# Performance work log

Measured on AMD Instinct MI355X. Metric: run time of the kernel, lower is better.

Reference implementation:

```python
import jax, jax.numpy as jnp
import numpy as np

B, C, W = 8, 128, 4096
REDUCTION = 8
D = C // REDUCTION  # 16


def setup_inputs() -> dict:
    key = jax.random.key(0)
    ks = jax.random.split(key, 7)
    scale = 0.05
    return {
        "x": jax.random.normal(ks[0], (B, C, W), dtype=jnp.float32),
        "Wq": jax.random.normal(ks[1], (D, C), dtype=jnp.float32) * scale,
        "bq": jax.random.normal(ks[2], (D,), dtype=jnp.float32) * scale,
        "Wk": jax.random.normal(ks[3], (D, C), dtype=jnp.float32) * scale,
        "bk": jax.random.normal(ks[4], (D,), dtype=jnp.float32) * scale,
        "Wv": jax.random.normal(ks[5], (C, C), dtype=jnp.float32) * scale,
        "bv": jax.random.normal(ks[6], (C,), dtype=jnp.float32) * scale,
    }


def reference(x, Wq, bq, Wk, bk, Wv, bv):
    # 1x1 Conv1d == per-position linear over channel axis
    q = jnp.einsum('dc,bcw->bdw', Wq, x) + bq[None, :, None]   # [B, D, W]
    k = jnp.einsum('dc,bcw->bdw', Wk, x) + bk[None, :, None]   # [B, D, W]
    v = jnp.einsum('oc,bcw->bow', Wv, x) + bv[None, :, None]   # [B, C, W]
    scale = D ** (-0.5)
    # scores[b,i,j] = q[b,:,i] . k[b,:,j]
    scores = jnp.einsum('bdi,bdj->bij', q, k) * scale          # [B, W, W]
    attn = jax.nn.softmax(scores, axis=-1)
    # torch.bmm(value, attn): context[b,c,w] = sum_j v[b,c,j] * attn[b,j,w]
    context = jnp.einsum('bcj,bjw->bcw', v, attn)              # [B, C, W]
    return context + x
```

## Files before the change

kernel.cpp:

```cpp
#include <hip/hip_runtime.h>

#define B_ 8
#define C_ 128
#define W_ 4096
#define D_ 16
#define SCALE2 0.3606737602222409f

typedef short bf16x8 __attribute__((ext_vector_type(8)));
typedef float f32x4 __attribute__((ext_vector_type(4)));
typedef float f32x16 __attribute__((ext_vector_type(16)));

__device__ __forceinline__ unsigned short f2bf(float f) {
    unsigned int u = __float_as_uint(f);
    u += 0x7fffu + ((u >> 16) & 1u);
    return (unsigned short)(u >> 16);
}
__device__ __forceinline__ float bf2f(unsigned short h) {
    return __uint_as_float(((unsigned int)h) << 16);
}
__device__ __forceinline__ unsigned int pk2bf(float lo, float hi) {
    return __builtin_amdgcn_perm(__float_as_uint(hi), __float_as_uint(lo), 0x07060302u);
}
__device__ __forceinline__ bf16x8 u4_to_bf8(unsigned int a, unsigned int b,
                                            unsigned int c, unsigned int d) {
    union { uint4 u; bf16x8 v; } t;
    t.u = make_uint4(a, b, c, d);
    return t.v;
}
__device__ __forceinline__ bf16x8 uint4_as_bf8(uint4 u) {
    union { uint4 u; bf16x8 v; } t;
    t.u = u;
    return t.v;
}
__device__ __forceinline__ bf16x8 exp2pack8(f32x16 s, int r0) {
    return u4_to_bf8(
        pk2bf(__builtin_amdgcn_exp2f(s[r0+0]), __builtin_amdgcn_exp2f(s[r0+1])),
        pk2bf(__builtin_amdgcn_exp2f(s[r0+2]), __builtin_amdgcn_exp2f(s[r0+3])),
        pk2bf(__builtin_amdgcn_exp2f(s[r0+4]), __builtin_amdgcn_exp2f(s[r0+5])),
        pk2bf(__builtin_amdgcn_exp2f(s[r0+6]), __builtin_amdgcn_exp2f(s[r0+7])));
}
__device__ __forceinline__ int xswz(int j, int c8) {
    return c8 ^ (j & 7) ^ ((j >> 3) & 7);
}

__global__ __launch_bounds__(256) void prep(
    const float* __restrict__ Wq, const float* __restrict__ Wk, const float* __restrict__ Wv,
    unsigned short* __restrict__ Wvbf, unsigned short* __restrict__ Wqkbf)
{
    int g = blockIdx.x * 256 + threadIdx.x;
    const float* src; unsigned short* dst; float sc = 1.0f;
    if (g < 4096)      { src = Wv + g * 4;            dst = Wvbf + g * 4; }
    else if (g < 4608) { int t = g - 4096; src = Wq + t * 4; dst = Wqkbf + t * 4; sc = SCALE2; }
    else               { int t = g - 4608; src = Wk + t * 4; dst = Wqkbf + 2048 + t * 4; }
    float4 v = *(const float4*)src;
    unsigned short h[4] = {f2bf(v.x * sc), f2bf(v.y * sc), f2bf(v.z * sc), f2bf(v.w * sc)};
    *(ushort4*)dst = *(ushort4*)h;
}

__global__ __launch_bounds__(256) void proj(
    const float* __restrict__ x, const unsigned short* __restrict__ Wvbf,
    const unsigned short* __restrict__ Wqkbf,
    const float* __restrict__ bqp, const float* __restrict__ bkp, const float* __restrict__ bvp,
    unsigned short* __restrict__ qws2, unsigned short* __restrict__ kws2,
    unsigned short* __restrict__ vws2)
{
    __shared__ unsigned short xbf[32 * 128];
    __shared__ unsigned short outs[128 * 36];
    __shared__ unsigned short qk_s[2][32][24];

    int b  = blockIdx.x & 7;
    int j0 = (blockIdx.x >> 3) * 32;
    int jt = j0 >> 5;
    int tid = threadIdx.x;
    int wid = tid >> 6, lane = tid & 63, n = lane & 15, q4 = lane >> 4;

    {
        unsigned int* xbf32 = (unsigned int*)xbf;
#pragma unroll
        for (int i = 0; i < 8; i++) {
            int p = tid + 256 * i;
            int c2 = p >> 5;
            int j  = p & 31;
            const float* xp = x + (size_t)(b * C_ + 2 * c2) * W_ + j0 + j;
            float lo = xp[0];
            float hi = xp[W_];
            xbf32[j * 64 + xswz(j, c2 >> 2) * 4 + (c2 & 3)] = pk2bf(lo, hi);
        }
    }
    __syncthreads();

    const f32x4 zero = {0.f, 0.f, 0.f, 0.f};
    f32x4 accv[2][2]; f32x4 accqk = zero;
#pragma unroll
    for (int os = 0; os < 2; os++)
#pragma unroll
        for (int js = 0; js < 2; js++) accv[os][js] = zero;

    int isK = wid >> 1;
    int jsm = wid & 1;

#pragma unroll
    for (int kk = 0; kk < 128; kk += 32) {
        bf16x8 av[2], aqkf, bx[2];
#pragma unroll
        for (int os = 0; os < 2; os++)
            av[os] = *(const bf16x8*)(Wvbf + (wid * 32 + os * 16 + n) * 128 + kk + q4 * 8);
        aqkf = *(const bf16x8*)(Wqkbf + (isK * 16 + n) * 128 + kk + q4 * 8);
#pragma unroll
        for (int js = 0; js < 2; js++) {
            int j = js * 16 + n;
            bx[js] = *(const bf16x8*)&xbf[j * 128 + xswz(j, (kk >> 3) + q4) * 8];
        }
#pragma unroll
        for (int os = 0; os < 2; os++)
#pragma unroll
            for (int js = 0; js < 2; js++)
                accv[os][js] = __builtin_amdgcn_mfma_f32_16x16x32_bf16(av[os], bx[js], accv[os][js], 0, 0, 0);
        accqk = __builtin_amdgcn_mfma_f32_16x16x32_bf16(aqkf, bx[jsm], accqk, 0, 0, 0);
    }

    {
        int pos = jsm * 16 + n;
        const float* bias = isK ? bkp : bqp;
        float bsc = isK ? 1.0f : SCALE2;
#pragma unroll
        for (int r = 0; r < 4; r++)
            qk_s[isK][pos][q4 * 4 + r] = f2bf(accqk[r] + bias[q4 * 4 + r] * bsc);
    }

    float bvv[2][4];
#pragma unroll
    for (int os = 0; os < 2; os++)
#pragma unroll
        for (int r = 0; r < 4; r++) bvv[os][r] = bvp[wid * 32 + os * 16 + q4 * 4 + r];
#pragma unroll
    for (int os = 0; os < 2; os++)
#pragma unroll
        for (int js = 0; js < 2; js++)
#pragma unroll
            for (int r = 0; r < 4; r++) {
                int c = wid * 32 + os * 16 + q4 * 4 + r;
                int j = js * 16 + n;
                outs[c * 36 + j] = f2bf(accv[os][js][r] + bvv[os][r]);
            }
    __syncthreads();

    if (tid < 128) {
        int qk = tid >> 6, hh = (tid >> 5) & 1, jl = tid & 31;
        uint4 v = *(const uint4*)&qk_s[qk][jl][hh * 8];
        unsigned short* dst = (qk ? kws2 : qws2)
            + (size_t)(b * 128 + jt) * 512 + hh * 256 + jl * 8;
        *(uint4*)dst = v;
    }
#pragma unroll
    for (int rep = 0; rep < 2; rep++) {
        int t = tid + rep * 256;
        int c = t & 127, sel = t >> 7;
        int jb = (sel >> 1) * 16 + (sel & 1) * 4;
        uint2 lo = *(const uint2*)&outs[c * 36 + jb];
        uint2 hi = *(const uint2*)&outs[c * 36 + jb + 8];
        *(uint4*)(vws2 + ((size_t)(b * 128 + jt) * 4 + sel) * 1024 + c * 8) =
            make_uint4(lo.x, lo.y, hi.x, hi.y);
    }
}

__global__ __launch_bounds__(256) void row_stats(
    const unsigned short* __restrict__ qws2, const unsigned short* __restrict__ kws2,
    float* __restrict__ rlp)
{
    int blk = blockIdx.x;
    int b = blk & 7;
    int j0 = ((blk >> 3) & 31) * 128;
    int wsp = blk >> 8;
    int tid = threadIdx.x;
    int wid = tid >> 6, lane = tid & 63, wl = lane & 31, h = lane >> 5;

    const unsigned short* qb = qws2 + (size_t)b * 65536;
    const unsigned short* kb = kws2 + (size_t)b * 65536;
    int jt = (j0 >> 5) + wid;

    bf16x8 aq = *(const bf16x8*)(qb + (size_t)jt * 512 + h * 256 + wl * 8);
    f32x16 zero16 = {0.f,0.f,0.f,0.f,0.f,0.f,0.f,0.f,0.f,0.f,0.f,0.f,0.f,0.f,0.f,0.f};

    float lt[16];
#pragma unroll
    for (int r = 0; r < 16; r++) lt[r] = 0.f;

    bf16x8 bkc = *(const bf16x8*)(kb + (size_t)(wsp * 32) * 512 + h * 256 + wl * 8);
    for (int t = 0; t < 32; t++) {
        f32x16 s = __builtin_amdgcn_mfma_f32_32x32x16_bf16(aq, bkc, zero16, 0, 0, 0);
        int tn = wsp * 32 + ((t + 1) & 31);
        bkc = *(const bf16x8*)(kb + (size_t)tn * 512 + h * 256 + wl * 8);
#pragma unroll
        for (int r = 0; r < 16; r++) lt[r] += __builtin_amdgcn_exp2f(s[r]);
    }
#pragma unroll
    for (int mask = 1; mask < 32; mask <<= 1)
#pragma unroll
        for (int r = 0; r < 16; r++) lt[r] += __shfl_xor(lt[r], mask, 64);
    if (wl == 0) {
#pragma unroll
        for (int g = 0; g < 4; g++) {
            f32x4 v = {lt[4*g+0], lt[4*g+1], lt[4*g+2], lt[4*g+3]};
            *(f32x4*)(rlp + (size_t)wsp * 32768 + (size_t)b * W_ + j0 + wid * 32 + 4 * h + 8 * g) = v;
        }
    }
}

__global__ __launch_bounds__(256) void finl(const float* __restrict__ rlp,
                                            float* __restrict__ rls)
{
    int g = blockIdx.x * 256 + threadIdx.x;
    float l = rlp[g] + rlp[32768 + g] + rlp[65536 + g] + rlp[98304 + g];
    rls[g] = 1.0f / l;
}

__global__ __launch_bounds__(256) void vscale(unsigned short* __restrict__ vws2,
                                              const float* __restrict__ rls)
{
    int g = blockIdx.x * 256 + threadIdx.x;
    int hh = (g >> 7) & 1, kf = (g >> 8) & 1, jt = (g >> 9) & 127, b = g >> 16;
    int jb = jt * 32 + kf * 16 + 4 * hh;
    const float* rp = rls + (size_t)b * W_ + jb;
    float4 r0 = *(const float4*)rp;
    float4 r1 = *(const float4*)(rp + 8);
    uint4 v = *(const uint4*)(vws2 + (size_t)g * 8);
    unsigned int o0 = pk2bf(bf2f((unsigned short)(v.x & 0xffffu)) * r0.x,
                            bf2f((unsigned short)(v.x >> 16))     * r0.y);
    unsigned int o1 = pk2bf(bf2f((unsigned short)(v.y & 0xffffu)) * r0.z,
                            bf2f((unsigned short)(v.y >> 16))     * r0.w);
    unsigned int o2 = pk2bf(bf2f((unsigned short)(v.z & 0xffffu)) * r1.x,
                            bf2f((unsigned short)(v.z >> 16))     * r1.y);
    unsigned int o3 = pk2bf(bf2f((unsigned short)(v.w & 0xffffu)) * r1.z,
                            bf2f((unsigned short)(v.w >> 16))     * r1.w);
    *(uint4*)(vws2 + (size_t)g * 8) = make_uint4(o0, o1, o2, o3);
}

__global__ __launch_bounds__(256, 2) void attn_out(
    const float* __restrict__ x, const unsigned short* __restrict__ qws2,
    const unsigned short* __restrict__ kws2, const unsigned short* __restrict__ vws2,
    float* __restrict__ out)
{
    __shared__ float red[2][128 * 68];

    int b  = blockIdx.x & 7;
    int w0 = (blockIdx.x >> 3) * 64;
    int tid = threadIdx.x;
    int wid = tid >> 6, lane = tid & 63, wl = lane & 31, h = lane >> 5;

    const unsigned short* qb  = qws2 + (size_t)b * 65536;
    const unsigned short* kb  = kws2 + (size_t)b * 65536;
    const unsigned short* vtb = vws2 + (size_t)b * 524288;

    bf16x8 bk0 = *(const bf16x8*)(kb + (size_t)((w0 >> 5) + 0) * 512 + h * 256 + wl * 8);
    bf16x8 bk1 = *(const bf16x8*)(kb + (size_t)((w0 >> 5) + 1) * 512 + h * 256 + wl * 8);

    f32x16 zero16 = {0.f,0.f,0.f,0.f,0.f,0.f,0.f,0.f,0.f,0.f,0.f,0.f,0.f,0.f,0.f,0.f};
    f32x16 acc[4][2];
#pragma unroll
    for (int mt = 0; mt < 4; mt++)
#pragma unroll
        for (int nt = 0; nt < 2; nt++) acc[mt][nt] = zero16;

    const int qoff = h * 256 + wl * 8;

    bf16x8 aq = *(const bf16x8*)(qb + (size_t)(wid) * 512 + qoff);
    uint4 vf[4][2];
#pragma unroll
    for (int mt = 0; mt < 4; mt++)
#pragma unroll
        for (int kf = 0; kf < 2; kf++)
            vf[mt][kf] = *(const uint4*)(vtb + (size_t)wid * 4096 + kf * 2048 + h * 1024 + (mt * 32 + wl) * 8);
    f32x16 s0 = __builtin_amdgcn_mfma_f32_32x32x16_bf16(aq, bk0, zero16, 0, 0, 0);
    f32x16 s1 = __builtin_amdgcn_mfma_f32_32x32x16_bf16(aq, bk1, zero16, 0, 0, 0);
    aq = *(const bf16x8*)(qb + (size_t)(4 + wid) * 512 + qoff);
    bf16x8 bfrag[2][2];
    bfrag[0][0] = exp2pack8(s0, 0); bfrag[1][0] = exp2pack8(s0, 8);
    bfrag[0][1] = exp2pack8(s1, 0); bfrag[1][1] = exp2pack8(s1, 8);

    for (int it = 0; it < 32; it++) {
        int jtn = ((it + 1) & 31) * 4 + wid;
        uint4 vfn[4][2];
#pragma unroll
        for (int mt = 0; mt < 4; mt++)
#pragma unroll
            for (int kf = 0; kf < 2; kf++)
                vfn[mt][kf] = *(const uint4*)(vtb + (size_t)jtn * 4096 + kf * 2048 + h * 1024 + (mt * 32 + wl) * 8);
#pragma unroll
        for (int mt = 0; mt < 4; mt++)
#pragma unroll
            for (int kf = 0; kf < 2; kf++) {
                bf16x8 af = uint4_as_bf8(vf[mt][kf]);
#pragma unroll
                for (int nt = 0; nt < 2; nt++)
                    acc[mt][nt] = __builtin_amdgcn_mfma_f32_32x32x16_bf16(af, bfrag[kf][nt], acc[mt][nt], 0, 0, 0);
            }
        s0 = __builtin_amdgcn_mfma_f32_32x32x16_bf16(aq, bk0, zero16, 0, 0, 0);
        s1 = __builtin_amdgcn_mfma_f32_32x32x16_bf16(aq, bk1, zero16, 0, 0, 0);
        aq = *(const bf16x8*)(qb + (size_t)(((it + 2) & 31) * 4 + wid) * 512 + qoff);
        bfrag[0][0] = exp2pack8(s0, 0); bfrag[1][0] = exp2pack8(s0, 8);
        bfrag[0][1] = exp2pack8(s1, 0); bfrag[1][1] = exp2pack8(s1, 8);
#pragma unroll
        for (int mt = 0; mt < 4; mt++)
#pragma unroll
            for (int kf = 0; kf < 2; kf++) vf[mt][kf] = vfn[mt][kf];
    }

#define WRITE_TILE(BUF)                                                           \
    {                                                                             \
        float* _b = (BUF);                                                        \
        _Pragma("unroll") for (int mt = 0; mt < 4; mt++)                          \
        _Pragma("unroll") for (int nt = 0; nt < 2; nt++)                          \
        _Pragma("unroll") for (int r = 0; r < 16; r++)                            \
            _b[(mt * 32 + (r & 3) + 8 * (r >> 2) + 4 * h) * 68 + nt * 32 + wl] = acc[mt][nt][r]; \
    }
#define ADD_TILE(BUF)                                                             \
    {                                                                             \
        const float* _b = (BUF);                                                  \
        _Pragma("unroll") for (int mt = 0; mt < 4; mt++)                          \
        _Pragma("unroll") for (int nt = 0; nt < 2; nt++)                          \
        _Pragma("unroll") for (int r = 0; r < 16; r++)                            \
            acc[mt][nt][r] += _b[(mt * 32 + (r & 3) + 8 * (r >> 2) + 4 * h) * 68 + nt * 32 + wl]; \
    }
    if (wid >= 2) WRITE_TILE(red[wid - 2]);
    __syncthreads();
    if (wid < 2) ADD_TILE(red[wid]);
    __syncthreads();
    if (wid == 1) WRITE_TILE(red[0]);
    __syncthreads();
    if (wid == 0) { ADD_TILE(red[0]); WRITE_TILE(red[0]); }
    __syncthreads();
#undef WRITE_TILE
#undef ADD_TILE

#pragma unroll
    for (int u = 0; u < 8; u++) {
        int k = tid + 256 * u;
        int c = k >> 4, wseg = (k & 15) * 4;
        size_t gidx = (size_t)(b * C_ + c) * W_ + w0 + wseg;
        float4 xv = *(const float4*)(x + gidx);
        const float* s = &red[0][c * 68 + wseg];
        float4 o = make_float4(s[0] + xv.x, s[1] + xv.y, s[2] + xv.z, s[3] + xv.w);
        *(float4*)(out + gidx) = o;
    }
}

extern "C" void kernel_launch(void* const* d_in, const int* in_sizes, int n_in,
                              void* d_out, int out_size, void* d_ws, size_t ws_size,
                              hipStream_t stream)
{
    const float* x  = (const float*)d_in[0];
    const float* Wq = (const float*)d_in[1];
    const float* bq = (const float*)d_in[2];
    const float* Wk = (const float*)d_in[3];
    const float* bk = (const float*)d_in[4];
    const float* Wv = (const float*)d_in[5];
    const float* bv = (const float*)d_in[6];
    float* out = (float*)d_out;

    unsigned short* qws2 = (unsigned short*)d_ws;
    unsigned short* kws2 = qws2 + (size_t)524288;
    unsigned short* vws2 = kws2 + (size_t)524288;
    unsigned short* Wvbf = vws2 + (size_t)4194304;
    unsigned short* Wqkbf = Wvbf + 16384;
    float* rlp = (float*)(Wqkbf + 4096);
    float* rls = rlp + 131072;

    prep<<<20, 256, 0, stream>>>(Wq, Wk, Wv, Wvbf, Wqkbf);
    proj<<<1024, 256, 0, stream>>>(x, Wvbf, Wqkbf, bq, bk, bv, qws2, kws2, vws2);
    row_stats<<<1024, 256, 0, stream>>>(qws2, kws2, rlp);
    finl<<<128, 256, 0, stream>>>(rlp, rls);
    vscale<<<2048, 256, 0, stream>>>(vws2, rls);
    attn_out<<<512, 256, 0, stream>>>(x, qws2, kws2, vws2, out);
}
```

Baseline: 160.1 us.

## Split attn_out work across 8 waves sharing P tiles via LDS

After: 158.3 us. No clear change (-1.2%).

```diff
diff --git a/kernel.cpp b/kernel.cpp
--- a/kernel.cpp
+++ b/kernel.cpp
@@ -32,8 +32,8 @@
     t.u = u;
     return t.v;
 }
-__device__ __forceinline__ bf16x8 exp2pack8(f32x16 s, int r0) {
-    return u4_to_bf8(
+__device__ __forceinline__ uint4 exp2pkq(f32x16 s, int r0) {
+    return make_uint4(
         pk2bf(__builtin_amdgcn_exp2f(s[r0+0]), __builtin_amdgcn_exp2f(s[r0+1])),
         pk2bf(__builtin_amdgcn_exp2f(s[r0+2]), __builtin_amdgcn_exp2f(s[r0+3])),
         pk2bf(__builtin_amdgcn_exp2f(s[r0+4]), __builtin_amdgcn_exp2f(s[r0+5])),
@@ -236,112 +236,105 @@
     *(uint4*)(vws2 + (size_t)g * 8) = make_uint4(o0, o1, o2, o3);
 }
 
-__global__ __launch_bounds__(256, 2) void attn_out(
+__global__ __launch_bounds__(512, 4) void attn_out(
     const float* __restrict__ x, const unsigned short* __restrict__ qws2,
     const unsigned short* __restrict__ kws2, const unsigned short* __restrict__ vws2,
     float* __restrict__ out)
 {
-    __shared__ float red[2][128 * 68];
+    __shared__ uint4 p_lds[2][1024];
+    __shared__ float red[128 * 68];
 
     int b  = blockIdx.x & 7;
     int w0 = (blockIdx.x >> 3) * 64;
     int tid = threadIdx.x;
     int wid = tid >> 6, lane = tid & 63, wl = lane & 31, h = lane >> 5;
+    int cq = wid >> 1, kh = wid & 1;
 
     const unsigned short* qb  = qws2 + (size_t)b * 65536;
     const unsigned short* kb  = kws2 + (size_t)b * 65536;
-    const unsigned short* vtb = vws2 + (size_t)b * 524288;
-
-    bf16x8 bk0 = *(const bf16x8*)(kb + (size_t)((w0 >> 5) + 0) * 512 + h * 256 + wl * 8);
-    bf16x8 bk1 = *(const bf16x8*)(kb + (size_t)((w0 >> 5) + 1) * 512 + h * 256 + wl * 8);
+    const uint4* vtb4 = (const uint4*)(vws2 + (size_t)b * 524288) + h * 128 + (cq * 32 + wl);
+    const int qoff = h * 256 + wl * 8;
+
+    bf16x8 bk = *(const bf16x8*)(kb + (size_t)((w0 >> 5) + kh) * 512 + h * 256 + wl * 8);
 
     f32x16 zero16 = {0.f,0.f,0.f,0.f,0.f,0.f,0.f,0.f,0.f,0.f,0.f,0.f,0.f,0.f,0.f,0.f};
-    f32x16 acc[4][2];
-#pragma unroll
-    for (int mt = 0; mt < 4; mt++)
-#pragma unroll
-        for (int nt = 0; nt < 2; nt++) acc[mt][nt] = zero16;
-
-    const int qoff = h * 256 + wl * 8;
-
-    bf16x8 aq = *(const bf16x8*)(qb + (size_t)(wid) * 512 + qoff);
-    uint4 vf[4][2];
-#pragma unroll
-    for (int mt = 0; mt < 4; mt++)
-#pragma unroll
-        for (int kf = 0; kf < 2; kf++)
-            vf[mt][kf] = *(const uint4*)(vtb + (size_t)wid * 4096 + kf * 2048 + h * 1024 + (mt * 32 + wl) * 8);
-    f32x16 s0 = __builtin_amdgcn_mfma_f32_32x32x16_bf16(aq, bk0, zero16, 0, 0, 0);
-    f32x16 s1 = __builtin_amdgcn_mfma_f32_32x32x16_bf16(aq, bk1, zero16, 0, 0, 0);
-    aq = *(const bf16x8*)(qb + (size_t)(4 + wid) * 512 + qoff);
-    bf16x8 bfrag[2][2];
-    bfrag[0][0] = exp2pack8(s0, 0); bfrag[1][0] = exp2pack8(s0, 8);
-    bfrag[0][1] = exp2pack8(s1, 0); bfrag[1][1] = exp2pack8(s1, 8);
-
+    f32x16 acc[2];
+    acc[0] = zero16; acc[1] = zero16;
+
+    const int wbase = cq * 256 + h * 64 + kh * 32 + wl;
+    const int rbase = kh * 512 + h * 64 + wl;
+
+    bf16x8 aq = *(const bf16x8*)(qb + (size_t)cq * 512 + qoff);
+    uint4 vf[4];
+#pragma unroll
+    for (int kf = 0; kf < 4; kf++)
+        vf[kf] = vtb4[(size_t)(kh * 4 + kf) * 256];
+    {
+        f32x16 s = __builtin_amdgcn_mfma_f32_32x32x16_bf16(aq, bk, zero16, 0, 0, 0);
+        aq = *(const bf16x8*)(qb + (size_t)(4 + cq) * 512 + qoff);
+        p_lds[0][wbase]       = exp2pkq(s, 0);
+        p_lds[0][wbase + 128] = exp2pkq(s, 8);
+    }
+    __syncthreads();
+
+#pragma unroll 2
     for (int it = 0; it < 32; it++) {
-        int jtn = ((it + 1) & 31) * 4 + wid;
-        uint4 vfn[4][2];
-#pragma unroll
-        for (int mt = 0; mt < 4; mt++)
-#pragma unroll
-            for (int kf = 0; kf < 2; kf++)
-                vfn[mt][kf] = *(const uint4*)(vtb + (size_t)jtn * 4096 + kf * 2048 + h * 1024 + (mt * 32 + wl) * 8);
-#pragma unroll
-        for (int mt = 0; mt < 4; mt++)
-#pragma unroll
-            for (int kf = 0; kf < 2; kf++) {
-                bf16x8 af = uint4_as_bf8(vf[mt][kf]);
-#pragma unroll
-                for (int nt = 0; nt < 2; nt++)
-                    acc[mt][nt] = __builtin_amdgcn_mfma_f32_32x32x16_bf16(af, bfrag[kf][nt], acc[mt][nt], 0, 0, 0);
+        int cur = it & 1, nxt = cur ^ 1;
+        uint4 vfn[4];
+#pragma unroll
+        for (int kf = 0; kf < 4; kf++) {
+            int kg = ((it + 1) & 31) * 8 + kh * 4 + kf;
+            vfn[kf] = vtb4[(size_t)kg * 256];
+        }
+        f32x16 s = __builtin_amdgcn_mfma_f32_32x32x16_bf16(aq, bk, zero16, 0, 0, 0);
+        aq = *(const bf16x8*)(qb + (size_t)(((it + 2) & 31) * 4 + cq) * 512 + qoff);
+        p_lds[nxt][wbase]       = exp2pkq(s, 0);
+        p_lds[nxt][wbase + 128] = exp2pkq(s, 8);
+        __builtin_amdgcn_s_setprio(1);
+#pragma unroll
+        for (int kf = 0; kf < 4; kf++) {
+            bf16x8 af = uint4_as_bf8(vf[kf]);
+#pragma unroll
+            for (int nt = 0; nt < 2; nt++) {
+                bf16x8 bp = uint4_as_bf8(p_lds[cur][rbase + kf * 128 + nt * 32]);
+                acc[nt] = __builtin_amdgcn_mfma_f32_32x32x16_bf16(af, bp, acc[nt], 0, 0, 0);
             }
-        s0 = __builtin_amdgcn_mfma_f32_32x32x16_bf16(aq, bk0, zero16, 0, 0, 0);
-        s1 = __builtin_amdgcn_mfma_f32_32x32x16_bf16(aq, bk1, zero16, 0, 0, 0);
-        aq = *(const bf16x8*)(qb + (size_t)(((it + 2) & 31) * 4 + wid) * 512 + qoff);
-        bfrag[0][0] = exp2pack8(s0, 0); bfrag[1][0] = exp2pack8(s0, 8);
-        bfrag[0][1] = exp2pack8(s1, 0); bfrag[1][1] = exp2pack8(s1, 8);
-#pragma unroll
-        for (int mt = 0; mt < 4; mt++)
-#pragma unroll
-            for (int kf = 0; kf < 2; kf++) vf[mt][kf] = vfn[mt][kf];
-    }
-
-#define WRITE_TILE(BUF)                                                           \
-    {                                                                             \
-        float* _b = (BUF);                                                        \
-        _Pragma("unroll") for (int mt = 0; mt < 4; mt++)                          \
-        _Pragma("unroll") for (int nt = 0; nt < 2; nt++)                          \
-        _Pragma("unroll") for (int r = 0; r < 16; r++)                            \
-            _b[(mt * 32 + (r & 3) + 8 * (r >> 2) + 4 * h) * 68 + nt * 32 + wl] = acc[mt][nt][r]; \
-    }
-#define ADD_TILE(BUF)                                                             \
-    {                                                                             \
-        const float* _b = (BUF);                                                  \
-        _Pragma("unroll") for (int mt = 0; mt < 4; mt++)                          \
-        _Pragma("unroll") for (int nt = 0; nt < 2; nt++)                          \
-        _Pragma("unroll") for (int r = 0; r < 16; r++)                            \
-            acc[mt][nt][r] += _b[(mt * 32 + (r & 3) + 8 * (r >> 2) + 4 * h) * 68 + nt * 32 + wl]; \
-    }
-    if (wid >= 2) WRITE_TILE(red[wid - 2]);
-    __syncthreads();
-    if (wid < 2) ADD_TILE(red[wid]);
-    __syncthreads();
-    if (wid == 1) WRITE_TILE(red[0]);
-    __syncthreads();
-    if (wid == 0) { ADD_TILE(red[0]); WRITE_TILE(red[0]); }
-    __syncthreads();
-#undef WRITE_TILE
-#undef ADD_TILE
-
-#pragma unroll
-    for (int u = 0; u < 8; u++) {
-        int k = tid + 256 * u;
+        }
+        __builtin_amdgcn_s_setprio(0);
+        __syncthreads();
+#pragma unroll
+        for (int kf = 0; kf < 4; kf++) vf[kf] = vfn[kf];
+    }
+
+#define CROW(r) (cq * 32 + ((r) & 3) + 8 * ((r) >> 2) + 4 * h)
+    if (kh == 1) {
+#pragma unroll
+        for (int nt = 0; nt < 2; nt++)
+#pragma unroll
+            for (int r = 0; r < 16; r++)
+                red[CROW(r) * 68 + nt * 32 + wl] = acc[nt][r];
+    }
+    __syncthreads();
+    if (kh == 0) {
+#pragma unroll
+        for (int nt = 0; nt < 2; nt++)
+#pragma unroll
+            for (int r = 0; r < 16; r++) {
+                int o = CROW(r) * 68 + nt * 32 + wl;
+                red[o] += acc[nt][r];
+            }
+    }
+#undef CROW
+    __syncthreads();
+
+#pragma unroll
+    for (int u = 0; u < 4; u++) {
+        int k = tid + 512 * u;
         int c = k >> 4, wseg = (k & 15) * 4;
         size_t gidx = (size_t)(b * C_ + c) * W_ + w0 + wseg;
         float4 xv = *(const float4*)(x + gidx);
-        const float* s = &red[0][c * 68 + wseg];
-        float4 o = make_float4(s[0] + xv.x, s[1] + xv.y, s[2] + xv.z, s[3] + xv.w);
-        *(float4*)(out + gidx) = o;
+        const float* sp = &red[c * 68 + wseg];
+        *(float4*)(out + gidx) = make_float4(sp[0] + xv.x, sp[1] + xv.y, sp[2] + xv.z, sp[3] + xv.w);
     }
 }
 
@@ -371,5 +364,5 @@
     row_stats<<<1024, 256, 0, stream>>>(qws2, kws2, rlp);
     finl<<<128, 256, 0, stream>>>(rlp, rls);
     vscale<<<2048, 256, 0, stream>>>(vws2, rls);
-    attn_out<<<512, 256, 0, stream>>>(x, qws2, kws2, vws2, out);
-}
+    attn_out<<<512, 512, 0, stream>>>(x, qws2, kws2, vws2, out);
+}
```
